# Kernel optimization log

Hardware: AMD Instinct MI355X
Metric: run time of the kernel (lower is better)

The kernel has to match this reference:

```python
import jax, jax.numpy as jnp
import numpy as np
from jax.scipy.special import gammaln

# ---- constants matching init_kwargs ----
D = 64            # num_nodes
K = 64            # DiBS latent rank (k = d default)
P = 32            # n_particles
N_MC = 16         # MC graph samples for score-function grad estimator
PROJ = 128        # proj_dims
N = 2048          # observations
H = 5.0           # h_latent (Frobenius squared-exponential kernel bandwidth)
ALPHA = 0.2       # alpha_linear * t  (single SVGD step)
STEP = 0.005      # SVGD step size
ALPHA_MU = 1.0
ALPHA_LAMBD = float(D + 2)
THETA_MU = 0.0
P_EDGE = 4.0 / (D - 1)          # Erdos-Renyi edge prob (~2 expected edges/node)
LATENT_STD = 1.0 / np.sqrt(K)   # DiBS default latent prior std


def bge_log_marginal(g, data, mu0, alpha_mu, alpha_lambd):
    """BGe log marginal likelihood log p(data | G) for 0/1 adjacency g [d,d]."""
    n, d = data.shape
    small_t = alpha_mu * (alpha_lambd - d - 1.0) / (alpha_mu + 1.0)
    xbar = data.mean(0)
    xc = data - xbar
    R = small_t * jnp.eye(d) + xc.T @ xc \
        + (n * alpha_mu / (n + alpha_mu)) * jnp.outer(xbar - mu0, xbar - mu0)

    def masked_slogdet(mask):  # logdet of R restricted to mask-selected rows/cols
        m = jnp.outer(mask, mask)
        return jnp.linalg.slogdet(m * R + (1.0 - m) * jnp.eye(d))[1]

    def node_score(j):
        parents = g[:, j].astype(R.dtype)
        pj = jnp.maximum(parents, (jnp.arange(d) == j).astype(R.dtype))
        l = jnp.sum(parents)
        log_gamma = (0.5 * (jnp.log(alpha_mu) - jnp.log(n + alpha_mu))
                     + gammaln(0.5 * (n + alpha_lambd - d + l + 1.0))
                     - gammaln(0.5 * (alpha_lambd - d + l + 1.0))
                     - 0.5 * n * jnp.log(jnp.pi)
                     + 0.5 * (alpha_lambd - d + 2.0 * l + 1.0) * jnp.log(small_t))
        return (log_gamma
                + 0.5 * (n + alpha_lambd - d + l) * masked_slogdet(parents)
                - 0.5 * (n + alpha_lambd - d + l + 1.0) * masked_slogdet(pj))

    return jnp.sum(jax.vmap(node_score)(jnp.arange(d)))


def _dense(key, fan_in, fan_out):
    return jax.random.normal(key, (fan_in, fan_out), jnp.float32) * 0.05


def setup_inputs() -> dict:
    key = jax.random.key(0)
    ks = jax.random.split(key, 16)
    return {
        "z_gt": jax.random.normal(ks[0], (N, D), jnp.float32),
        "init_particles_z": jax.random.normal(ks[1], (P, D, K, 2), jnp.float32) * LATENT_STD,
        "enc_w0": _dense(ks[2], D * D, 20), "enc_b0": jnp.zeros(20, jnp.float32),
        "enc_w1": _dense(ks[3], 20, D),     "enc_b1": jnp.zeros(D, jnp.float32),
        "enc_w2": _dense(ks[4], D, D),      "enc_b2": jnp.zeros(D, jnp.float32),
        "mu_w0": _dense(ks[5], D, D), "mu_b0": jnp.zeros(D, jnp.float32),
        "mu_w1": _dense(ks[6], D, D), "mu_b1": jnp.zeros(D, jnp.float32),
        "lv_w0": _dense(ks[7], D, D), "lv_b0": jnp.zeros(D, jnp.float32),
        "lv_w1": _dense(ks[8], D, D), "lv_b1": jnp.zeros(D, jnp.float32),
        "dec_w0": _dense(ks[9], D, 10),       "dec_b0": jnp.zeros(10, jnp.float32),
        "dec_w1": _dense(ks[10], 10, PROJ),   "dec_b1": jnp.zeros(PROJ, jnp.float32),
        "dec_w2": _dense(ks[11], PROJ, PROJ), "dec_b2": jnp.zeros(PROJ, jnp.float32),
        "seed": 0,
    }


def reference(z_gt, init_particles_z, enc_w0, enc_b0, enc_w1, enc_b1, enc_w2, enc_b2,
              mu_w0, mu_b0, mu_w1, mu_b1, lv_w0, lv_b0, lv_w1, lv_b1,
              dec_w0, dec_b0, dec_w1, dec_b1, dec_w2, dec_b2, seed):
    key = jax.random.key(seed)
    d = z_gt.shape[1]
    od = 1.0 - jnp.eye(d)
    z = init_particles_z                                   # [P,d,k,2]
    u, v = z[..., 0], z[..., 1]
    scores = jnp.einsum('pik,pjk->pij', u, v)              # [P,d,d]
    probs = jax.nn.sigmoid(ALPHA * scores) * od            # soft graph, zero diag

    # --- score-function estimate of grad_z log E_G[p(data|G)] (DiBS marginal) ---
    key, sk = jax.random.split(key)
    gs = jax.random.bernoulli(sk, probs[:, None], (P, N_MC, d, d)).astype(z.dtype) * od
    mu0_inf = jnp.zeros(d, z.dtype)
    logp = jax.vmap(jax.vmap(
        lambda g: bge_log_marginal(g, z_gt, mu0_inf, 1.0, d + 2.0)))(gs)   # [P,S]
    w = jax.nn.softmax(logp, axis=1)                       # self-normalized weights
    M = ALPHA * (gs - probs[:, None]) * od                 # d log q(G|Z) / d scores
    grad_u = jnp.einsum('ps,psij,pjk->pik', w, M, v)
    grad_v = jnp.einsum('ps,psij,pik->pjk', w, M, u)

    # --- grad of soft-graph ER prior + Gaussian latent prior ---
    logit_pe = jnp.log(P_EDGE) - jnp.log1p(-P_EDGE)
    Mp = ALPHA * probs * (1.0 - probs) * logit_pe * od
    grad_u = grad_u + jnp.einsum('pij,pjk->pik', Mp, v) - u / (LATENT_STD ** 2)
    grad_v = grad_v + jnp.einsum('pij,pik->pjk', Mp, u) - v / (LATENT_STD ** 2)
    grads = jnp.stack([grad_u, grad_v], axis=-1)           # [P,d,k,2]

    # --- one SVGD step with Frobenius squared-exponential kernel ---
    zf = z.reshape(P, -1)
    gf = grads.reshape(P, -1)
    sq = jnp.sum((zf[:, None] - zf[None]) ** 2, -1)
    Kmat = jnp.exp(-sq / H)                                # symmetric [P,P]
    rep = (-2.0 / H) * (Kmat @ zf - zf * Kmat.sum(1, keepdims=True))
    z_new = z + STEP * ((Kmat @ gf + rep) / P).reshape(z.shape)

    # --- hard graphs: particle_to_g_lim (alpha -> inf) ---
    s2 = jnp.einsum('pik,pjk->pij', z_new[..., 0], z_new[..., 1])
    g_hard = (s2 > 0).astype(z.dtype) * od                 # [P,d,d]

    mu0_bge = jnp.full(d, THETA_MU, z.dtype)
    log_p_z_given_g = jax.vmap(
        lambda g: bge_log_marginal(g, z_gt, mu0_bge, ALPHA_MU, ALPHA_LAMBD))(g_hard)

    # --- q(z | G) encoder (batched over particles) ---
    gf2 = g_hard.reshape(g_hard.shape[0], d * d)
    h = jax.nn.relu(gf2 @ enc_w0 + enc_b0)
    h = jax.nn.relu(h @ enc_w1 + enc_b1)
    h = jax.nn.relu(h @ enc_w2 + enc_b2)
    q_mu = jax.nn.relu(h @ mu_w0 + mu_b0) @ mu_w1 + mu_b1
    q_lv = jax.nn.relu(h @ lv_w0 + lv_b0) @ lv_w1 + lv_b1

    key, rk = jax.random.split(key)
    eps = jax.random.normal(rk, q_lv.shape, q_lv.dtype)
    q_z = q_mu + eps * jnp.exp(0.5 * q_lv)                 # reparameterize

    # --- decoder ---
    hdec = jax.nn.relu(q_z @ dec_w0 + dec_b0)
    hdec = jax.nn.relu(hdec @ dec_w1 + dec_b1)
    recons = hdec @ dec_w2 + dec_b2                        # [P, PROJ]

    return recons, log_p_z_given_g, q_z, q_mu, q_lv, g_hard, z_new
```

## Files before the change

### kernel.cpp

```cpp
#include <hip/hip_runtime.h>
#include <stdint.h>
#include <math.h>

typedef unsigned long long u64;
typedef unsigned int u32;
typedef unsigned short u16;

#define C_P 32
#define C_S 16
#define C_D 64
#define C_N 2048

#define R_OFF      0
#define CTAB_OFF   4160
#define KEYS_OFF   4224
#define PROBS_OFF  4232
#define GROW_OFF   135304
#define GCOL_OFF   168072
#define NS_OFF     200840
#define W_OFF      233608
#define GF_OFF     234120
#define KM_OFF     365192
#define ZN_OFF     365704
#define NS2_OFF    496776

#define WL_LIST0 16

#define HBLK 768
#define TB1 1280
#define TB0 2112
#define TB2 1312
#define E_H  (HBLK)
#define E_1  (E_H + TB1)
#define E_0  (E_1 + TB0)
#define NBLK_ALL (E_0 + TB2)

#define O_REC   0
#define O_LOGP  4096
#define O_QZ    4128
#define O_QMU   6176
#define O_QLV   8224
#define O_GH    10272
#define O_ZN    141344
#define O_TOTAL 403488

__device__ __forceinline__ void tf2x32(u32 k0, u32 k1, u32 x0, u32 x1,
                                       u32& o0, u32& o1) {
  u32 ks2 = k0 ^ k1 ^ 0x1BD11BDAu;
  x0 += k0; x1 += k1;
#define TFR(r) { x0 += x1; x1 = (x1 << r) | (x1 >> (32 - r)); x1 ^= x0; }
  TFR(13) TFR(15) TFR(26) TFR(6)   x0 += k1;  x1 += ks2 + 1u;
  TFR(17) TFR(29) TFR(16) TFR(24)  x0 += ks2; x1 += k0 + 2u;
  TFR(13) TFR(15) TFR(26) TFR(6)   x0 += k0;  x1 += k1 + 3u;
  TFR(17) TFR(29) TFR(16) TFR(24)  x0 += k1;  x1 += ks2 + 4u;
  TFR(13) TFR(15) TFR(26) TFR(6)   x0 += ks2; x1 += k0 + 5u;
#undef TFR
  o0 = x0; o1 = x1;
}

__device__ __forceinline__ double d_erfinv(double x) {
  double w = -log1p(-x * x);
  double p;
  if (w < 5.0) {
    w -= 2.5;
    p = 2.81022636e-08;
    p = 3.43273939e-07  + p * w;
    p = -3.5233877e-06  + p * w;
    p = -4.39150654e-06 + p * w;
    p = 0.00021858087   + p * w;
    p = -0.00125372503  + p * w;
    p = -0.00417768164  + p * w;
    p = 0.246640727     + p * w;
    p = 1.50140941      + p * w;
  } else {
    w = sqrt(w) - 3.0;
    p = -0.000200214257;
    p = 0.000100950558  + p * w;
    p = 0.00134934322   + p * w;
    p = -0.00367342844  + p * w;
    p = 0.00573950773   + p * w;
    p = -0.0076224613   + p * w;
    p = 0.00943887047   + p * w;
    p = 1.00167406      + p * w;
    p = 2.83297682      + p * w;
  }
  return p * x;
}

__device__ __forceinline__ double stirl(double z) {
  double zi = 1.0 / z;
  double zi2 = zi * zi;
  double s = (z - 0.5) * log(z) - z + 0.9189385332046727;
  s += zi * (1.0 / 12.0 - zi2 * (1.0 / 360.0 - zi2 * (1.0 / 1260.0)));
  return s;
}

__global__ void k_init(const float* x, const float* z, double* ws, const int* seedp) {
  int t = threadIdx.x;
  if (blockIdx.x < 64) {
    __shared__ double pS[8][64], pX[8][64];
    __shared__ double xbar[64];
    int j = blockIdx.x;
    int i = t & 63, c = t >> 6;
    if (j == 0) {
      if (t < 64) {
        int l = t;
        double term = (l >= 2) ? log((2049.0 + (double)l) / (4.0 * (1.0 + (double)l)))
                               : 0.0;
        double v = term;
#pragma unroll
        for (int off = 2; off <= 32; off <<= 1) {
          double o = __shfl_up(v, off, 64);
          if (l >= off) v += o;
        }
        const double LOG_HALF = -0.6931471805599453;
        double c0 = -0.5 * log(2049.0)
                  - 1024.0 * log(3.14159265358979323846);
        double seed = (l & 1)
          ? c0 + stirl(1026.0) + 2.5 * LOG_HALF
          : c0 + stirl(1025.5) + 0.12078223763524522235 + 1.5 * LOG_HALF;
        ws[CTAB_OFF + l] = seed + v;
      }
      if (t < 8) ((u32*)(ws + GF_OFF))[t] = 0;
      if (t == 0) {
        u32 kk0 = 0u, kk1 = (u32)seedp[0];
        u32 a0, a1, s0, s1, r0, r1, d0, d1;
        tf2x32(kk0, kk1, 0u, 0u, a0, a1);
        tf2x32(kk0, kk1, 0u, 1u, s0, s1);
        tf2x32(a0, a1, 0u, 0u, d0, d1); (void)d0; (void)d1;
        tf2x32(a0, a1, 0u, 1u, r0, r1);
        u32* keys = (u32*)(ws + KEYS_OFF);
        keys[0] = s0; keys[1] = s1; keys[2] = r0; keys[3] = r1;
      }
    }
    double sx = 0.0, sxx = 0.0;
    for (int n = c * 256; n < (c + 1) * 256; n++) {
      double xi = (double)x[n * 64 + i];
      double xj = (double)x[n * 64 + j];
      sx += xi; sxx += xi * xj;
    }
    pS[c][i] = sx; pX[c][i] = sxx;
    __syncthreads();
    if (t < 64) {
      double S = 0.0, X = 0.0;
      for (int cc = 0; cc < 8; cc++) { S += pS[cc][i]; X += pX[cc][i]; }
      xbar[i] = S / 2048.0;
      pX[0][i] = X;
    }
    __syncthreads();
    if (t < 64) {
      double xbi = xbar[i], xbj = xbar[j];
      double s = pX[0][i] - 2048.0 * xbi * xbj + (2048.0 / 2049.0) * xbi * xbj;
      if (i == j) s += 0.5;
      ((float*)(ws + R_OFF))[i * 64 + j] = (float)s;
    }
  } else {
    __shared__ float V[64 * 65];
    __shared__ float us[8][64];
    float* probs = (float*)(ws + PROBS_OFF);
    int b2 = blockIdx.x - 64;
    int p = b2 >> 3;
    int i = (b2 & 7) * 8 + (t >> 6);
    int j = t & 63, w = t >> 6;
    for (int jj = w; jj < 64; jj += 8)
      V[jj * 65 + j] = z[((p * 64 + jj) * 64 + j) * 2 + 1];
    us[w][j] = z[((p * 64 + i) * 64 + j) * 2 + 0];
    __syncthreads();
    float s = 0.f;
    for (int kk = 0; kk < 64; kk++)
      s += us[w][kk] * V[j * 65 + kk];
    float pr = (i == j) ? 0.f : 1.f / (1.f + expf(-0.2f * s));
    probs[(p * 64 + i) * 64 + j] = pr;
  }
}

__global__ void k_sample(double* ws) {
  const float* probs = (const float*)(ws + PROBS_OFF);
  const u32* keys = (const u32*)(ws + KEYS_OFF);
  u64* grow = (u64*)(ws + GROW_OFF);
  u64* gcol = (u64*)(ws + GCOL_OFF);
  u32* wl = (u32*)(ws + GF_OFF);
  int ps = blockIdx.x;
  int p = ps >> 4;
  int j = threadIdx.x;
  u32 k0 = keys[0], k1 = keys[1];
  u64 colmask = 0;
  for (int i = 0; i < 64; i++) {
    u32 lin = (u32)(ps * 4096 + i * 64 + j);
    u32 o0, o1; tf2x32(k0, k1, 0u, lin, o0, o1);
    u32 bits = o0 ^ o1;
    float f = __uint_as_float((bits >> 9) | 0x3f800000u) - 1.0f;
    bool bit = (f < probs[(p * 64 + i) * 64 + j]);
    u64 rm = __ballot(bit);
    if (j == 0) grow[ps * 64 + i] = rm;
    if (bit) colmask |= (1ull << i);
  }
  gcol[ps * 64 + j] = colmask;
  int m = (int)__popcll(colmask) + 1;
  int tier = (m <= 32) ? 0 : (m <= 36) ? 1 : (m <= 40) ? 2 : 3;
#pragma unroll
  for (int t = 0; t < 4; t++) {
    u64 b = __ballot(tier == t);
    if (tier == t) {
      int leader = (int)__builtin_ctzll(b);
      u32 off = (u32)__popcll(b & ((1ull << j) - 1ull));
      u32 base = 0;
      if (j == leader) base = atomicAdd(&wl[t], (u32)__popcll(b));
      base = (u32)__shfl((int)base, leader, 64);
      wl[WL_LIST0 + t * 32768 + base + off] = (u32)(ps * 64 + j);
    }
  }
}

__device__ __forceinline__ float rdlane(float x, int l) {
  return __uint_as_float(__builtin_amdgcn_readlane(__float_as_uint(x), (u32)l));
}

template<int MMAX>
__device__ __forceinline__ void tier_body2(const float* Rf, const double* ctab,
                                           const u64* masks, double* nodescore,
                                           const u32* wl, int tier,
                                           u32 brel, u32 nb, int (*idx)[2][64]) {
  int w = threadIdx.x >> 6;
  int lane = threadIdx.x & 63;
  u32 cnt = wl[tier];
  const u32* list = wl + WL_LIST0 + tier * 32768;
  u32 npair = (cnt + 1) >> 1;
  for (u32 ti = brel * 4 + (u32)w; ti < npair; ti += nb * 4) {
    u32 iA = 2 * ti, iB = iA + 1;
    bool hasB = (iB < cnt);
    int taskA = (int)list[iA];
    int taskB = (int)list[hasB ? iB : iA];
    u64 maskA = masks[taskA];
    u64 maskB = masks[taskB];
    int PA = (int)__popcll(maskA), PB = (int)__popcll(maskB);
    idx[w][0][lane] = 0;
    idx[w][1][lane] = 0;
    __builtin_amdgcn_wave_barrier();
    {
      u64 belowA = maskA & ((1ull << lane) - 1ull);
      if ((maskA >> lane) & 1ull) idx[w][0][(int)__popcll(belowA)] = lane;
      if (lane == 0) idx[w][0][PA] = taskA & 63;
      u64 belowB = maskB & ((1ull << lane) - 1ull);
      if ((maskB >> lane) & 1ull) idx[w][1][(int)__popcll(belowB)] = lane;
      if (lane == 0) idx[w][1][PB] = taskB & 63;
    }
    __builtin_amdgcn_wave_barrier();
    int rowA = idx[w][0][lane];
    int rowB = idx[w][1][lane];
    float va[MMAX], vb[MMAX];
#pragma unroll
    for (int c = 0; c < MMAX; c++) {
      va[c] = Rf[idx[w][0][c] * 64 + rowA];
      vb[c] = Rf[idx[w][1][c] * 64 + rowB];
    }
    float pivA = 1.0f, pivB = 1.0f;
#pragma unroll
    for (int k = 0; k < MMAX; k++) {
      float dkA = rdlane(va[k], k);
      float dkB = rdlane(vb[k], k);
      if (lane == k) { pivA = dkA; pivB = dkB; }
      float nsA = -va[k] * __builtin_amdgcn_rcpf(dkA);
      float nsB = -vb[k] * __builtin_amdgcn_rcpf(dkB);
#pragma unroll
      for (int b2 = k + 1; b2 < MMAX; b2++) {
        va[b2] += nsA * rdlane(va[k], b2);
        vb[b2] += nsB * rdlane(vb[k], b2);
      }
    }
    {
      int mA = PA + 1;
      float lastd = __shfl(pivA, PA, 64);
      float lv = (lane < mA) ? __logf(pivA) : 0.f;
      for (int off = 32; off > 0; off >>= 1) lv += __shfl_down(lv, off, 64);
      if (lane == 0) {
        double l = (double)PA;
        nodescore[taskA] = ctab[PA]
                         - 0.5 * (2050.0 + l) * (double)__logf(lastd)
                         - 0.5 * (double)lv;
      }
    }
    if (hasB) {
      int mB = PB + 1;
      float lastd = __shfl(pivB, PB, 64);
      float lv = (lane < mB) ? __logf(pivB) : 0.f;
      for (int off = 32; off > 0; off >>= 1) lv += __shfl_down(lv, off, 64);
      if (lane == 0) {
        double l = (double)PB;
        nodescore[taskB] = ctab[PB]
                         - 0.5 * (2050.0 + l) * (double)__logf(lastd)
                         - 0.5 * (double)lv;
      }
    }
    __builtin_amdgcn_wave_barrier();
  }
}

template<int MMAX>
__device__ __forceinline__ void tier_body(const float* Rf, const double* ctab,
                                          const u64* masks, double* nodescore,
                                          const u32* wl, int tier,
                                          u32 brel, u32 nb, int (*idx)[64]) {
  int w = threadIdx.x >> 6;
  int lane = threadIdx.x & 63;
  u32 cnt = wl[tier];
  const u32* list = wl + WL_LIST0 + tier * 32768;
  for (u32 ti = brel * 4 + (u32)w; ti < cnt; ti += nb * 4) {
    int task = (int)list[ti];
    int j = task & 63;
    u64 mask = masks[task];
    int P = (int)__popcll(mask);
    int m = P + 1;
    idx[w][lane] = 0;
    __builtin_amdgcn_wave_barrier();
    u64 below = mask & ((1ull << lane) - 1ull);
    if ((mask >> lane) & 1ull) idx[w][(int)__popcll(below)] = lane;
    if (lane == 0) idx[w][P] = j;
    __builtin_amdgcn_wave_barrier();
    int myrow = idx[w][lane];
    float v[MMAX];
#pragma unroll
    for (int c = 0; c < MMAX; c++)
      v[c] = Rf[idx[w][c] * 64 + myrow];
    float mypiv = 1.0f;
#pragma unroll
    for (int k = 0; k < MMAX; k++) {
      if (k < m) {
        float dk = rdlane(v[k], k);
        if (lane == k) mypiv = dk;
        float ns = -v[k] * __builtin_amdgcn_rcpf(dk);
#pragma unroll
        for (int b = k + 1; b < MMAX; b++)
          v[b] += ns * rdlane(v[k], b);
      }
    }
    float lastd = __shfl(mypiv, P, 64);
    float lv = (lane < m) ? __logf(mypiv) : 0.f;
    for (int off = 32; off > 0; off >>= 1) lv += __shfl_down(lv, off, 64);
    if (lane == 0) {
      double l = (double)P;
      nodescore[task] = ctab[P]
                      - 0.5 * (2050.0 + l) * (double)__logf(lastd)
                      - 0.5 * (double)lv;
    }
    __builtin_amdgcn_wave_barrier();
  }
}

#define WB() __builtin_amdgcn_wave_barrier()

__device__ void heavy_body(const float* Rf, const double* ctab,
                           const u64* masks, double* nodescore,
                           const u32* wl, u32 brel, u32 nb,
                           float* T, int* idx) {
  if (threadIdx.x >= 64) return;
  int lane = threadIdx.x;
  u32 cnt = wl[3];
  const u32* list = wl + WL_LIST0 + 3 * 32768;
  for (u32 ii = brel; ii < cnt; ii += nb) {
    WB();
    int task = (int)list[ii];
    int j = task & 63;
    u64 mask = masks[task];
    int P = (int)__popcll(mask);
    int m = P + 1;
    u64 below = mask & ((1ull << lane) - 1ull);
    if ((mask >> lane) & 1ull) idx[(int)__popcll(below)] = lane;
    if (lane == 0) idx[P] = j;
    WB();
    int trLane = (lane * (lane + 1)) >> 1;
    if (lane < m) {
      int cidx = idx[lane];
      int tr = 0;
      for (int r = 0; r < m; r++) {
        if (lane <= r) T[tr + lane] = Rf[idx[r] * 64 + cidx];
        tr += r + 1;
      }
    }
    WB();
    float mypiv = 1.0f, lastd = 1.0f;
    float v[40];
#pragma unroll
    for (int c = 0; c < 40; c++)
      v[c] = T[trLane + c];
#pragma unroll
    for (int k = 0; k < 40; k++) {
      if (k < m) {
        float dk = rdlane(v[k], k);
        if (lane == k) mypiv = dk;
        lastd = dk;
        float ns = -v[k] * __builtin_amdgcn_rcpf(dk);
#pragma unroll
        for (int b = k + 1; b < 40; b++)
          v[b] += ns * rdlane(v[k], b);
      }
    }
    if (m > 40) {
      for (int b = 40; b < m; b++) {
        float acc = 0.f;
#pragma unroll
        for (int k = 0; k < 40; k++) {
          float dk = rdlane(v[k], k);
          float abk = rdlane(v[k], b);
          acc += v[k] * abk * __builtin_amdgcn_rcpf(dk);
        }
        if (lane >= b) T[trLane + b] -= acc;
      }
      WB();
      for (int k = 40; k < m; k++) {
        float dk = T[((k * (k + 1)) >> 1) + k];
        if (lane == k) mypiv = dk;
        lastd = dk;
        float sk = T[trLane + k] * __builtin_amdgcn_rcpf(dk);
        for (int b = k + 1; b < m; b++) {
          float abk = T[((b * (b + 1)) >> 1) + k];
          if (lane >= b) T[trLane + b] -= sk * abk;
        }
        WB();
      }
    }
    double vv = (lane < m) ? log((double)mypiv) : 0.0;
    for (int off = 32; off > 0; off >>= 1) vv += __shfl_down(vv, off, 64);
    if (lane == 0) {
      double logB = vv;
      double logA = logB - log((double)lastd);
      double l = (double)P;
      nodescore[task] = ctab[P]
                      + 0.5 * (2050.0 + l) * logA
                      - 0.5 * (2051.0 + l) * logB;
    }
  }
}

__global__ __launch_bounds__(256) void k_chol_all(const float* Rf, const double* ctab,
                                                  const u64* masks, double* nodescore,
                                                  const u32* wl) {
  __shared__ int idx2[4][2][64];
  __shared__ int idx4[4][64];
  __shared__ float T[2080];
  __shared__ int idxh[64];
  u32 b = blockIdx.x;
  if (b < E_H)      heavy_body(Rf, ctab, masks, nodescore, wl, b, HBLK, T, idxh);
  else if (b < E_1) tier_body2<36>(Rf, ctab, masks, nodescore, wl, 1, b - E_H, TB1, idx2);
  else if (b < E_0) tier_body2<32>(Rf, ctab, masks, nodescore, wl, 0, b - E_1, TB0, idx2);
  else              tier_body<40>(Rf, ctab, masks, nodescore, wl, 2, b - E_0, TB2, idx4);
}

template<bool TRANSPOSE>
__global__ __launch_bounds__(64) void k_chol(const float* Rf, const double* ctab,
                                             const u64* masks, double* nodescore) {
  __shared__ float T[2080];
  __shared__ int idx[64];
  int task = blockIdx.x;
  int j = task & 63;
  int lane = threadIdx.x;
  u64 mask;
  if (TRANSPOSE) {
    int p = task >> 6;
    u64 rm = masks[p * 64 + lane];
    mask = __ballot((rm >> j) & 1ull);
  } else {
    mask = masks[task];
  }
  int P = (int)__popcll(mask);
  int m = P + 1;
  u64 below = mask & ((1ull << lane) - 1ull);
  if ((mask >> lane) & 1ull) idx[(int)__popcll(below)] = lane;
  if (lane == 0) idx[P] = j;
  __syncthreads();
  int trLane = (lane * (lane + 1)) >> 1;
  if (lane < m) {
    int cidx = idx[lane];
    int tr = 0;
    for (int r = 0; r < m; r++) {
      if (lane <= r) T[tr + lane] = Rf[idx[r] * 64 + cidx];
      tr += r + 1;
    }
  }
  __syncthreads();
  float mypiv = 1.0f, lastd = 1.0f;
  float v[40];
#pragma unroll
  for (int c = 0; c < 40; c++)
    v[c] = T[trLane + c];
#pragma unroll
  for (int k = 0; k < 40; k++) {
    if (k < m) {
      float dk = rdlane(v[k], k);
      if (lane == k) mypiv = dk;
      lastd = dk;
      float ns = -v[k] * __builtin_amdgcn_rcpf(dk);
#pragma unroll
      for (int b = k + 1; b < 40; b++)
        v[b] += ns * rdlane(v[k], b);
    }
  }
  if (m > 40) {
    for (int b = 40; b < m; b++) {
      float acc = 0.f;
#pragma unroll
      for (int k = 0; k < 40; k++) {
        float dk = rdlane(v[k], k);
        float abk = rdlane(v[k], b);
        acc += v[k] * abk * __builtin_amdgcn_rcpf(dk);
      }
      if (lane >= b) T[trLane + b] -= acc;
    }
    __syncthreads();
    for (int k = 40; k < m; k++) {
      float dk = T[((k * (k + 1)) >> 1) + k];
      if (lane == k) mypiv = dk;
      lastd = dk;
      float sk = T[trLane + k] * __builtin_amdgcn_rcpf(dk);
      for (int b = k + 1; b < m; b++) {
        float abk = T[((b * (b + 1)) >> 1) + k];
        if (lane >= b) T[trLane + b] -= sk * abk;
      }
      __syncthreads();
    }
  }
  double vv = (lane < m) ? log((double)mypiv) : 0.0;
  for (int off = 32; off > 0; off >>= 1) vv += __shfl_down(vv, off, 64);
  if (lane == 0) {
    double logB = vv;
    double logA = logB - log((double)lastd);
    double l = (double)P;
    nodescore[task] = ctab[P]
                    + 0.5 * (2050.0 + l) * logA
                    - 0.5 * (2051.0 + l) * logB;
  }
}

__global__ void k_grad(double* ws, const float* z) {
  const float* probs = (const float*)(ws + PROBS_OFF);
  const u64* grow = (const u64*)(ws + GROW_OFF);
  const u64* gcol = (const u64*)(ws + GCOL_OFF);
  const double* ns = ws + NS_OFF;
  float* gf = (float*)(ws + GF_OFF);
  const float LOGIT = -2.6903717578966254f;
  int bb = blockIdx.x;
  int k = threadIdx.x;
  __shared__ float acc[64];
  __shared__ double part[64];
  __shared__ double wsh[16];
  if (bb < 4096) {
    int p = (bb < 2048) ? (bb >> 6) : ((bb - 2048) >> 6);
    {
      int s = k & 15, c = k >> 4;
      double a2 = 0.0;
      for (int j2 = c * 16; j2 < (c + 1) * 16; j2++)
        a2 += ns[(p * 16 + s) * 64 + j2];
      part[k] = a2;
      __syncthreads();
      if (k < 16) part[k] = part[k] + part[k + 16] + part[k + 32] + part[k + 48];
      __syncthreads();
      if (k == 0) {
        double m2 = part[0];
        for (int s2 = 1; s2 < 16; s2++) m2 = fmax(m2, part[s2]);
        double e[16], sum = 0.0;
        for (int s2 = 0; s2 < 16; s2++) { e[s2] = exp(part[s2] - m2); sum += e[s2]; }
        for (int s2 = 0; s2 < 16; s2++) wsh[s2] = e[s2] / sum;
      }
      __syncthreads();
    }
    if (bb < 2048) {
      int i = bb & 63;
      float gb = 0.f, wsum = 0.f;
      for (int s = 0; s < 16; s++) {
        float wv = (float)wsh[s];
        wsum += wv;
        gb += wv * (float)((grow[(p * 16 + s) * 64 + i] >> k) & 1ull);
      }
      float pr = probs[(p * 64 + i) * 64 + k];
      float od = (i == k) ? 0.f : 1.f;
      acc[k] = (0.2f * (gb - pr * wsum) + 0.2f * pr * (1.f - pr) * LOGIT) * od;
      __syncthreads();
      float s = 0.f;
      for (int j = 0; j < 64; j++)
        s += acc[j] * z[((p * 64 + j) * 64 + k) * 2 + 1];
      s -= 64.f * z[((p * 64 + i) * 64 + k) * 2 + 0];
      gf[p * 8192 + (i * 64 + k) * 2 + 0] = s;
    } else {
      int j = (bb - 2048) & 63;
      float gb = 0.f, wsum = 0.f;
      for (int s = 0; s < 16; s++) {
        float wv = (float)wsh[s];
        wsum += wv;
        gb += wv * (float)((gcol[(p * 16 + s) * 64 + j] >> k) & 1ull);
      }
      float pr = probs[(p * 64 + k) * 64 + j];
      float od = (k == j) ? 0.f : 1.f;
      acc[k] = (0.2f * (gb - pr * wsum) + 0.2f * pr * (1.f - pr) * LOGIT) * od;
      __syncthreads();
      float s = 0.f;
      for (int i = 0; i < 64; i++)
        s += acc[i] * z[((p * 64 + i) * 64 + k) * 2 + 0];
      s -= 64.f * z[((p * 64 + j) * 64 + k) * 2 + 1];
      gf[p * 8192 + (j * 64 + k) * 2 + 1] = s;
    }
  } else {
    float* Km = (float*)(ws + KM_OFF);
    int b = bb - 4096;
    int a = b >> 5, b2 = b & 31;
    float accf = 0.f;
    for (int d0 = k; d0 < 8192; d0 += 64) {
      float diff = z[a * 8192 + d0] - z[b2 * 8192 + d0];
      accf += diff * diff;
    }
    for (int off = 32; off > 0; off >>= 1) accf += __shfl_down(accf, off, 64);
    if (k == 0) Km[a * 32 + b2] = expf(-accf / 5.0f);
  }
}

__global__ void k_znew(const float* z, double* ws, float* out) {
  const float* Km = (const float*)(ws + KM_OFF);
  const float* gf = (const float*)(ws + GF_OFF);
  float* zn = (float*)(ws + ZN_OFF);
  int gid = blockIdx.x * 64 + threadIdx.x;
  int p = gid >> 13, t = gid & 8191;
  float zp = z[p * 8192 + t];
  float accg = 0.f, accz = 0.f, ks = 0.f;
  for (int b = 0; b < 32; b++) {
    float kv = Km[p * 32 + b];
    accg += kv * gf[b * 8192 + t];
    accz += kv * z[b * 8192 + t];
    ks += kv;
  }
  float rep = -0.4f * (accz - zp * ks);
  float v = zp + 0.005f * ((accg + rep) / 32.f);
  zn[p * 8192 + t] = v;
  out[O_ZN + p * 8192 + t] = v;
}

__global__ __launch_bounds__(64) void k_s2col(double* ws, float* out) {
  const float* zn = (const float*)(ws + ZN_OFF);
  u64* grow2 = (u64*)(ws + NS_OFF);
  int b = blockIdx.x; int p = b >> 6, i = b & 63;
  int j = threadIdx.x;
  __shared__ float V[64 * 65];
  __shared__ float us[64];
  int k = j;
  us[k] = zn[p * 8192 + (i * 64 + k) * 2 + 0];
  for (int jj = 0; jj < 64; jj++)
    V[jj * 65 + k] = zn[p * 8192 + (jj * 64 + k) * 2 + 1];
  __syncthreads();
  float s = 0.f;
  for (int kk = 0; kk < 64; kk++)
    s += us[kk] * V[j * 65 + kk];
  bool bit = (i != j) && (s > 0.0f);
  out[O_GH + (p * 64 + i) * 64 + j] = bit ? 1.0f : 0.0f;
  u64 m = __ballot(bit);
  if (j == 0) grow2[p * 64 + i] = m;
}

__global__ __launch_bounds__(256) void k_mlp(double* ws, float* out, const double* ns2,
    const float* ew0, const float* eb0, const float* ew1, const float* eb1,
    const float* ew2, const float* eb2,
    const float* mw0, const float* mb0, const float* mw1, const float* mb1,
    const float* lw0, const float* lb0, const float* lw1, const float* lb1,
    const float* dw0, const float* db0, const float* dw1, const float* db1,
    const float* dw2, const float* db2) {
  int p = blockIdx.x, t = threadIdx.x;
  int w = t >> 6, lane = t & 63;
  const u64* grow2 = (const u64*)(ws + NS_OFF);
  const u32* keys = (const u32*)(ws + KEYS_OFF);
  __shared__ float pt[4][64];
  __shared__ float e0p[4][20];
  __shared__ float h0[20], h1[64], h2[64], hm[64], hl[64];
  __shared__ float qmu[64], qlv[64], qz[64], h3[10], h4[128];

  if (w == 0) {
    double vv = ns2[p * 64 + lane];
    for (int off = 32; off > 0; off >>= 1) vv += __shfl_down(vv, off, 64);
    if (lane == 0) out[O_LOGP + p] = (float)vv;
  }

  {
    int i = t >> 2;
    int jb = (t & 3) * 16;
    u32 m16 = (u32)((grow2[p * 64 + i] >> jb) & 0xFFFFull);
    float acc[20];
#pragma unroll
    for (int o = 0; o < 20; o++) acc[o] = 0.f;
    const float4* wb = (const float4*)(ew0 + (size_t)(t * 16) * 20);
#pragma unroll
    for (int q = 0; q < 16; q++) {
      float mq = (float)((m16 >> q) & 1u);
      float4 r0 = wb[q * 5 + 0], r1 = wb[q * 5 + 1], r2 = wb[q * 5 + 2];
      float4 r3 = wb[q * 5 + 3], r4 = wb[q * 5 + 4];
      acc[0]  += mq * r0.x; acc[1]  += mq * r0.y; acc[2]  += mq * r0.z; acc[3]  += mq * r0.w;
      acc[4]  += mq * r1.x; acc[5]  += mq * r1.y; acc[6]  += mq * r1.z; acc[7]  += mq * r1.w;
      acc[8]  += mq * r2.x; acc[9]  += mq * r2.y; acc[10] += mq * r2.z; acc[11] += mq * r2.w;
      acc[12] += mq * r3.x; acc[13] += mq * r3.y; acc[14] += mq * r3.z; acc[15] += mq * r3.w;
      acc[16] += mq * r4.x; acc[17] += mq * r4.y; acc[18] += mq * r4.z; acc[19] += mq * r4.w;
    }
#pragma unroll
    for (int o = 0; o < 20; o++) {
      float v = acc[o];
      for (int off = 32; off > 0; off >>= 1) v += __shfl_down(v, off, 64);
      if (lane == 0) e0p[w][o] = v;
    }
  }
  __syncthreads();
  if (t < 20)
    h0[t] = fmaxf(eb0[t] + e0p[0][t] + e0p[1][t] + e0p[2][t] + e0p[3][t], 0.f);
  __syncthreads();

  {
    float s = 0.f;
#pragma unroll
    for (int q = 0; q < 5; q++) s += h0[w * 5 + q] * ew1[(w * 5 + q) * 64 + lane];
    pt[w][lane] = s;
  }
  __syncthreads();
  if (w == 0)
    h1[lane] = fmaxf(eb1[lane] + pt[0][lane] + pt[1][lane] + pt[2][lane] + pt[3][lane], 0.f);
  __syncthreads();

  {
    float s = 0.f;
#pragma unroll
    for (int q = 0; q < 16; q++) s += h1[w * 16 + q] * ew2[(w * 16 + q) * 64 + lane];
    pt[w][lane] = s;
  }
  __syncthreads();
  if (w == 0)
    h2[lane] = fmaxf(eb2[lane] + pt[0][lane] + pt[1][lane] + pt[2][lane] + pt[3][lane], 0.f);
  __syncthreads();

  {
    const float* W = (w < 2) ? mw0 : lw0;
    int qb = (w & 1) * 32;
    float s = 0.f;
#pragma unroll
    for (int q = 0; q < 32; q++) s += h2[qb + q] * W[(qb + q) * 64 + lane];
    pt[w][lane] = s;
  }
  __syncthreads();
  if (w == 0) hm[lane] = fmaxf(mb0[lane] + pt[0][lane] + pt[1][lane], 0.f);
  if (w == 1) hl[lane] = fmaxf(lb0[lane] + pt[2][lane] + pt[3][lane], 0.f);
  __syncthreads();

  {
    const float* W = (w < 2) ? mw1 : lw1;
    const float* src = (w < 2) ? hm : hl;
    int qb = (w & 1) * 32;
    float s = 0.f;
#pragma unroll
    for (int q = 0; q < 32; q++) s += src[qb + q] * W[(qb + q) * 64 + lane];
    pt[w][lane] = s;
  }
  __syncthreads();
  if (w == 0) qmu[lane] = mb1[lane] + pt[0][lane] + pt[1][lane];
  if (w == 1) qlv[lane] = lb1[lane] + pt[2][lane] + pt[3][lane];
  __syncthreads();

  if (w == 0) {
    u32 o0, o1;
    tf2x32(keys[2], keys[3], 0u, (u32)(p * 64 + lane), o0, o1);
    u32 bits = o0 ^ o1;
    float f = __uint_as_float((bits >> 9) | 0x3f800000u) - 1.0f;
    float LOF = __uint_as_float(0xBF7FFFFFu);
    float uu = fmaxf(LOF, f * 2.0f + LOF);
    float eps = (float)(1.4142135623730951 * d_erfinv((double)uu));
    float qzv = qmu[lane] + eps * expf(0.5f * qlv[lane]);
    qz[lane] = qzv;
    out[O_QZ  + p * 64 + lane] = qzv;
    out[O_QMU + p * 64 + lane] = qmu[lane];
    out[O_QLV + p * 64 + lane] = qlv[lane];
  }
  __syncthreads();

  {
    float s = 0.f;
    if (lane < 10) {
#pragma unroll
      for (int q = 0; q < 16; q++) s += qz[w * 16 + q] * dw0[(w * 16 + q) * 10 + lane];
    }
    pt[w][lane] = s;
  }
  __syncthreads();
  if (w == 0 && lane < 10)
    h3[lane] = fmaxf(db0[lane] + pt[0][lane] + pt[1][lane] + pt[2][lane] + pt[3][lane], 0.f);
  __syncthreads();

  {
    int o = (w >> 1) * 64 + lane;
    int qb = (w & 1) * 5;
    float s = 0.f;
#pragma unroll
    for (int q = 0; q < 5; q++) s += h3[qb + q] * dw1[(qb + q) * 128 + o];
    pt[w][lane] = s;
  }
  __syncthreads();
  if (w == 0) h4[lane]      = fmaxf(db1[lane]      + pt[0][lane] + pt[1][lane], 0.f);
  if (w == 1) h4[64 + lane] = fmaxf(db1[64 + lane] + pt[2][lane] + pt[3][lane], 0.f);
  __syncthreads();

  {
    int o = (w >> 1) * 64 + lane;
    int qb = (w & 1) * 64;
    float s = 0.f;
#pragma unroll
    for (int q = 0; q < 64; q++) s += h4[qb + q] * dw2[(qb + q) * 128 + o];
    pt[w][lane] = s;
  }
  __syncthreads();
  if (w == 0) out[O_REC + p * 128 + lane]      = db2[lane]      + pt[0][lane] + pt[1][lane];
  if (w == 1) out[O_REC + p * 128 + 64 + lane] = db2[64 + lane] + pt[2][lane] + pt[3][lane];
}

extern "C" void kernel_launch(void* const* d_in, const int* in_sizes, int n_in,
                              void* d_out, int out_size, void* d_ws, size_t ws_size,
                              hipStream_t stream) {
  (void)in_sizes; (void)n_in; (void)out_size; (void)ws_size;
  const float* z_gt = (const float*)d_in[0];
  const float* z0   = (const float*)d_in[1];
  const float* ew0 = (const float*)d_in[2];  const float* eb0 = (const float*)d_in[3];
  const float* ew1 = (const float*)d_in[4];  const float* eb1 = (const float*)d_in[5];
  const float* ew2 = (const float*)d_in[6];  const float* eb2 = (const float*)d_in[7];
  const float* mw0 = (const float*)d_in[8];  const float* mb0 = (const float*)d_in[9];
  const float* mw1 = (const float*)d_in[10]; const float* mb1 = (const float*)d_in[11];
  const float* lw0 = (const float*)d_in[12]; const float* lb0 = (const float*)d_in[13];
  const float* lw1 = (const float*)d_in[14]; const float* lb1 = (const float*)d_in[15];
  const float* dw0 = (const float*)d_in[16]; const float* db0 = (const float*)d_in[17];
  const float* dw1 = (const float*)d_in[18]; const float* db1 = (const float*)d_in[19];
  const float* dw2 = (const float*)d_in[20]; const float* db2 = (const float*)d_in[21];
  const int* seed = (const int*)d_in[22];
  double* ws = (double*)d_ws;
  float* out = (float*)d_out;
  const float* Rf = (const float*)(ws + R_OFF);
  const u32* wl = (const u32*)(ws + GF_OFF);

  k_init<<<320, 512, 0, stream>>>(z_gt, z0, ws, seed);
  k_sample<<<C_P * C_S, 64, 0, stream>>>(ws);
  k_chol_all<<<NBLK_ALL, 256, 0, stream>>>(Rf, ws + CTAB_OFF,
      (const u64*)(ws + GCOL_OFF), ws + NS_OFF, wl);
  k_grad<<<2 * C_P * C_D + C_P * C_P, 64, 0, stream>>>(ws, z0);
  k_znew<<<(C_P * 8192) / 64, 64, 0, stream>>>(z0, ws, out);
  k_s2col<<<C_P * C_D, 64, 0, stream>>>(ws, out);
  k_chol<true><<<C_P * C_D, 64, 0, stream>>>(Rf, ws + CTAB_OFF,
      (const u64*)(ws + NS_OFF), ws + NS2_OFF);
  k_mlp<<<C_P, 256, 0, stream>>>(ws, out, ws + NS2_OFF,
      ew0, eb0, ew1, eb1, ew2, eb2,
      mw0, mb0, mw1, mb1, lw0, lb0, lw1, lb1,
      dw0, db0, dw1, db1, dw2, db2);
}
```

Baseline: 329.3 us.

## Fuse graph sampling into init, move kernel matrix into Cholesky launch

The Bernoulli graph-sampling kernel is merged into k_init. Each block now computes a particle's full edge-probability matrix in shared memory and samples 8 MC graphs from it, recomputing the sampling key locally instead of reading it from the workspace. The SVGD kernel-matrix computation moves from k_grad into extra blocks of k_chol_all, and k_s2col switches to 512-thread blocks handling 8 rows each. The aim is fewer launches and less tail latency, at the cost of duplicated probability computation and a hipMemset that replaces the in-kernel worklist reset.

```diff
diff --git a/kernel.cpp b/kernel.cpp
--- a/kernel.cpp
+++ b/kernel.cpp
@@ -33,7 +33,9 @@
 #define E_H  (HBLK)
 #define E_1  (E_H + TB1)
 #define E_0  (E_1 + TB0)
-#define NBLK_ALL (E_0 + TB2)
+#define E_2  (E_0 + TB2)
+#define KMB  256
+#define NBLK_ALL (E_2 + KMB)
 
 #define O_REC   0
 #define O_LOGP  4096
@@ -96,10 +98,12 @@
 }
 
 __global__ void k_init(const float* x, const float* z, double* ws, const int* seedp) {
+  __shared__ double smem[6208];
   int t = threadIdx.x;
   if (blockIdx.x < 64) {
-    __shared__ double pS[8][64], pX[8][64];
-    __shared__ double xbar[64];
+    double* pS = smem;
+    double* pX = smem + 512;
+    double* xbar = smem + 1024;
     int j = blockIdx.x;
     int i = t & 63, c = t >> 6;
     if (j == 0) {
@@ -121,7 +125,6 @@
           : c0 + stirl(1025.5) + 0.12078223763524522235 + 1.5 * LOG_HALF;
         ws[CTAB_OFF + l] = seed + v;
       }
-      if (t < 8) ((u32*)(ws + GF_OFF))[t] = 0;
       if (t == 0) {
         u32 kk0 = 0u, kk1 = (u32)seedp[0];
         u32 a0, a1, s0, s1, r0, r1, d0, d1;
@@ -139,75 +142,76 @@
       double xj = (double)x[n * 64 + j];
       sx += xi; sxx += xi * xj;
     }
-    pS[c][i] = sx; pX[c][i] = sxx;
+    pS[c * 64 + i] = sx; pX[c * 64 + i] = sxx;
     __syncthreads();
     if (t < 64) {
       double S = 0.0, X = 0.0;
-      for (int cc = 0; cc < 8; cc++) { S += pS[cc][i]; X += pX[cc][i]; }
+      for (int cc = 0; cc < 8; cc++) { S += pS[cc * 64 + i]; X += pX[cc * 64 + i]; }
       xbar[i] = S / 2048.0;
-      pX[0][i] = X;
+      pX[i] = X;
     }
     __syncthreads();
     if (t < 64) {
       double xbi = xbar[i], xbj = xbar[j];
-      double s = pX[0][i] - 2048.0 * xbi * xbj + (2048.0 / 2049.0) * xbi * xbj;
+      double s = pX[i] - 2048.0 * xbi * xbj + (2048.0 / 2049.0) * xbi * xbj;
       if (i == j) s += 0.5;
       ((float*)(ws + R_OFF))[i * 64 + j] = (float)s;
     }
   } else {
-    __shared__ float V[64 * 65];
-    __shared__ float us[8][64];
+    float* V  = (float*)smem;
+    float* U  = V + 64 * 65;
+    float* PL = U + 64 * 65;
     float* probs = (float*)(ws + PROBS_OFF);
-    int b2 = blockIdx.x - 64;
-    int p = b2 >> 3;
-    int i = (b2 & 7) * 8 + (t >> 6);
+    u64* grow = (u64*)(ws + GROW_OFF);
+    u64* gcol = (u64*)(ws + GCOL_OFF);
+    u32* wl = (u32*)(ws + GF_OFF);
+    int sidx = blockIdx.x - 64;
+    int p = sidx >> 1, half = sidx & 1;
     int j = t & 63, w = t >> 6;
-    for (int jj = w; jj < 64; jj += 8)
+    for (int jj = w; jj < 64; jj += 8) {
       V[jj * 65 + j] = z[((p * 64 + jj) * 64 + j) * 2 + 1];
-    us[w][j] = z[((p * 64 + i) * 64 + j) * 2 + 0];
-    __syncthreads();
-    float s = 0.f;
-    for (int kk = 0; kk < 64; kk++)
-      s += us[w][kk] * V[j * 65 + kk];
-    float pr = (i == j) ? 0.f : 1.f / (1.f + expf(-0.2f * s));
-    probs[(p * 64 + i) * 64 + j] = pr;
-  }
-}
-
-__global__ void k_sample(double* ws) {
-  const float* probs = (const float*)(ws + PROBS_OFF);
-  const u32* keys = (const u32*)(ws + KEYS_OFF);
-  u64* grow = (u64*)(ws + GROW_OFF);
-  u64* gcol = (u64*)(ws + GCOL_OFF);
-  u32* wl = (u32*)(ws + GF_OFF);
-  int ps = blockIdx.x;
-  int p = ps >> 4;
-  int j = threadIdx.x;
-  u32 k0 = keys[0], k1 = keys[1];
-  u64 colmask = 0;
-  for (int i = 0; i < 64; i++) {
-    u32 lin = (u32)(ps * 4096 + i * 64 + j);
-    u32 o0, o1; tf2x32(k0, k1, 0u, lin, o0, o1);
-    u32 bits = o0 ^ o1;
-    float f = __uint_as_float((bits >> 9) | 0x3f800000u) - 1.0f;
-    bool bit = (f < probs[(p * 64 + i) * 64 + j]);
-    u64 rm = __ballot(bit);
-    if (j == 0) grow[ps * 64 + i] = rm;
-    if (bit) colmask |= (1ull << i);
-  }
-  gcol[ps * 64 + j] = colmask;
-  int m = (int)__popcll(colmask) + 1;
-  int tier = (m <= 32) ? 0 : (m <= 36) ? 1 : (m <= 40) ? 2 : 3;
-#pragma unroll
-  for (int t = 0; t < 4; t++) {
-    u64 b = __ballot(tier == t);
-    if (tier == t) {
-      int leader = (int)__builtin_ctzll(b);
-      u32 off = (u32)__popcll(b & ((1ull << j) - 1ull));
-      u32 base = 0;
-      if (j == leader) base = atomicAdd(&wl[t], (u32)__popcll(b));
-      base = (u32)__shfl((int)base, leader, 64);
-      wl[WL_LIST0 + t * 32768 + base + off] = (u32)(ps * 64 + j);
+      U[jj * 65 + j] = z[((p * 64 + jj) * 64 + j) * 2 + 0];
+    }
+    __syncthreads();
+#pragma unroll
+    for (int r = 0; r < 8; r++) {
+      int i = w * 8 + r;
+      float s = 0.f;
+      for (int kk = 0; kk < 64; kk++)
+        s += U[i * 65 + kk] * V[j * 65 + kk];
+      float pr = (i == j) ? 0.f : 1.f / (1.f + expf(-0.2f * s));
+      PL[i * 64 + j] = pr;
+      if (half == 0) probs[(p * 64 + i) * 64 + j] = pr;
+    }
+    __syncthreads();
+    int ps = p * 16 + half * 8 + w;
+    u32 kk1 = (u32)seedp[0];
+    u32 k0, k1; tf2x32(0u, kk1, 0u, 1u, k0, k1);
+    u64 colmask = 0;
+    for (int i = 0; i < 64; i++) {
+      u32 lin = (u32)(ps * 4096 + i * 64 + j);
+      u32 o0, o1; tf2x32(k0, k1, 0u, lin, o0, o1);
+      u32 bits = o0 ^ o1;
+      float f = __uint_as_float((bits >> 9) | 0x3f800000u) - 1.0f;
+      bool bit = (f < PL[i * 64 + j]);
+      u64 rm = __ballot(bit);
+      if (j == 0) grow[ps * 64 + i] = rm;
+      if (bit) colmask |= (1ull << i);
+    }
+    gcol[ps * 64 + j] = colmask;
+    int m = (int)__popcll(colmask) + 1;
+    int tier = (m <= 32) ? 0 : (m <= 36) ? 1 : (m <= 40) ? 2 : 3;
+#pragma unroll
+    for (int tt = 0; tt < 4; tt++) {
+      u64 b = __ballot(tier == tt);
+      if (tier == tt) {
+        int leader = (int)__builtin_ctzll(b);
+        u32 off = (u32)__popcll(b & ((1ull << j) - 1ull));
+        u32 base = 0;
+        if (j == leader) base = atomicAdd(&wl[tt], (u32)__popcll(b));
+        base = (u32)__shfl((int)base, leader, 64);
+        wl[WL_LIST0 + tt * 32768 + base + off] = (u32)(ps * 64 + j);
+      }
     }
   }
 }
@@ -434,7 +438,8 @@
 
 __global__ __launch_bounds__(256) void k_chol_all(const float* Rf, const double* ctab,
                                                   const u64* masks, double* nodescore,
-                                                  const u32* wl) {
+                                                  const u32* wl, const float* z,
+                                                  float* Km) {
   __shared__ int idx2[4][2][64];
   __shared__ int idx4[4][64];
   __shared__ float T[2080];
@@ -443,7 +448,19 @@
   if (b < E_H)      heavy_body(Rf, ctab, masks, nodescore, wl, b, HBLK, T, idxh);
   else if (b < E_1) tier_body2<36>(Rf, ctab, masks, nodescore, wl, 1, b - E_H, TB1, idx2);
   else if (b < E_0) tier_body2<32>(Rf, ctab, masks, nodescore, wl, 0, b - E_1, TB0, idx2);
-  else              tier_body<40>(Rf, ctab, masks, nodescore, wl, 2, b - E_0, TB2, idx4);
+  else if (b < E_2) tier_body<40>(Rf, ctab, masks, nodescore, wl, 2, b - E_0, TB2, idx4);
+  else {
+    int pair = (int)(b - E_2) * 4 + (threadIdx.x >> 6);
+    int lane = threadIdx.x & 63;
+    int a = pair >> 5, b2 = pair & 31;
+    float accf = 0.f;
+    for (int d0 = lane; d0 < 8192; d0 += 64) {
+      float diff = z[a * 8192 + d0] - z[b2 * 8192 + d0];
+      accf += diff * diff;
+    }
+    for (int off = 32; off > 0; off >>= 1) accf += __shfl_down(accf, off, 64);
+    if (lane == 0) Km[a * 32 + b2] = expf(-accf / 5.0f);
+  }
 }
 
 template<bool TRANSPOSE>
@@ -543,72 +560,59 @@
   __shared__ float acc[64];
   __shared__ double part[64];
   __shared__ double wsh[16];
-  if (bb < 4096) {
-    int p = (bb < 2048) ? (bb >> 6) : ((bb - 2048) >> 6);
-    {
-      int s = k & 15, c = k >> 4;
-      double a2 = 0.0;
-      for (int j2 = c * 16; j2 < (c + 1) * 16; j2++)
-        a2 += ns[(p * 16 + s) * 64 + j2];
-      part[k] = a2;
-      __syncthreads();
-      if (k < 16) part[k] = part[k] + part[k + 16] + part[k + 32] + part[k + 48];
-      __syncthreads();
-      if (k == 0) {
-        double m2 = part[0];
-        for (int s2 = 1; s2 < 16; s2++) m2 = fmax(m2, part[s2]);
-        double e[16], sum = 0.0;
-        for (int s2 = 0; s2 < 16; s2++) { e[s2] = exp(part[s2] - m2); sum += e[s2]; }
-        for (int s2 = 0; s2 < 16; s2++) wsh[s2] = e[s2] / sum;
-      }
-      __syncthreads();
-    }
-    if (bb < 2048) {
-      int i = bb & 63;
-      float gb = 0.f, wsum = 0.f;
-      for (int s = 0; s < 16; s++) {
-        float wv = (float)wsh[s];
-        wsum += wv;
-        gb += wv * (float)((grow[(p * 16 + s) * 64 + i] >> k) & 1ull);
-      }
-      float pr = probs[(p * 64 + i) * 64 + k];
-      float od = (i == k) ? 0.f : 1.f;
-      acc[k] = (0.2f * (gb - pr * wsum) + 0.2f * pr * (1.f - pr) * LOGIT) * od;
-      __syncthreads();
-      float s = 0.f;
-      for (int j = 0; j < 64; j++)
-        s += acc[j] * z[((p * 64 + j) * 64 + k) * 2 + 1];
-      s -= 64.f * z[((p * 64 + i) * 64 + k) * 2 + 0];
-      gf[p * 8192 + (i * 64 + k) * 2 + 0] = s;
-    } else {
-      int j = (bb - 2048) & 63;
-      float gb = 0.f, wsum = 0.f;
-      for (int s = 0; s < 16; s++) {
-        float wv = (float)wsh[s];
-        wsum += wv;
-        gb += wv * (float)((gcol[(p * 16 + s) * 64 + j] >> k) & 1ull);
-      }
-      float pr = probs[(p * 64 + k) * 64 + j];
-      float od = (k == j) ? 0.f : 1.f;
-      acc[k] = (0.2f * (gb - pr * wsum) + 0.2f * pr * (1.f - pr) * LOGIT) * od;
-      __syncthreads();
-      float s = 0.f;
-      for (int i = 0; i < 64; i++)
-        s += acc[i] * z[((p * 64 + i) * 64 + k) * 2 + 0];
-      s -= 64.f * z[((p * 64 + j) * 64 + k) * 2 + 1];
-      gf[p * 8192 + (j * 64 + k) * 2 + 1] = s;
-    }
+  int p = (bb < 2048) ? (bb >> 6) : ((bb - 2048) >> 6);
+  {
+    int s = k & 15, c = k >> 4;
+    double a2 = 0.0;
+    for (int j2 = c * 16; j2 < (c + 1) * 16; j2++)
+      a2 += ns[(p * 16 + s) * 64 + j2];
+    part[k] = a2;
+    __syncthreads();
+    if (k < 16) part[k] = part[k] + part[k + 16] + part[k + 32] + part[k + 48];
+    __syncthreads();
+    if (k == 0) {
+      double m2 = part[0];
+      for (int s2 = 1; s2 < 16; s2++) m2 = fmax(m2, part[s2]);
+      double e[16], sum = 0.0;
+      for (int s2 = 0; s2 < 16; s2++) { e[s2] = exp(part[s2] - m2); sum += e[s2]; }
+      for (int s2 = 0; s2 < 16; s2++) wsh[s2] = e[s2] / sum;
+    }
+    __syncthreads();
+  }
+  if (bb < 2048) {
+    int i = bb & 63;
+    float gb = 0.f, wsum = 0.f;
+    for (int s = 0; s < 16; s++) {
+      float wv = (float)wsh[s];
+      wsum += wv;
+      gb += wv * (float)((grow[(p * 16 + s) * 64 + i] >> k) & 1ull);
+    }
+    float pr = probs[(p * 64 + i) * 64 + k];
+    float od = (i == k) ? 0.f : 1.f;
+    acc[k] = (0.2f * (gb - pr * wsum) + 0.2f * pr * (1.f - pr) * LOGIT) * od;
+    __syncthreads();
+    float s = 0.f;
+    for (int j = 0; j < 64; j++)
+      s += acc[j] * z[((p * 64 + j) * 64 + k) * 2 + 1];
+    s -= 64.f * z[((p * 64 + i) * 64 + k) * 2 + 0];
+    gf[p * 8192 + (i * 64 + k) * 2 + 0] = s;
   } else {
-    float* Km = (float*)(ws + KM_OFF);
-    int b = bb - 4096;
-    int a = b >> 5, b2 = b & 31;
-    float accf = 0.f;
-    for (int d0 = k; d0 < 8192; d0 += 64) {
-      float diff = z[a * 8192 + d0] - z[b2 * 8192 + d0];
-      accf += diff * diff;
-    }
-    for (int off = 32; off > 0; off >>= 1) accf += __shfl_down(accf, off, 64);
-    if (k == 0) Km[a * 32 + b2] = expf(-accf / 5.0f);
+    int j = (bb - 2048) & 63;
+    float gb = 0.f, wsum = 0.f;
+    for (int s = 0; s < 16; s++) {
+      float wv = (float)wsh[s];
+      wsum += wv;
+      gb += wv * (float)((gcol[(p * 16 + s) * 64 + j] >> k) & 1ull);
+    }
+    float pr = probs[(p * 64 + k) * 64 + j];
+    float od = (k == j) ? 0.f : 1.f;
+    acc[k] = (0.2f * (gb - pr * wsum) + 0.2f * pr * (1.f - pr) * LOGIT) * od;
+    __syncthreads();
+    float s = 0.f;
+    for (int i = 0; i < 64; i++)
+      s += acc[i] * z[((p * 64 + i) * 64 + k) * 2 + 0];
+    s -= 64.f * z[((p * 64 + j) * 64 + k) * 2 + 1];
+    gf[p * 8192 + (j * 64 + k) * 2 + 1] = s;
   }
 }
 
@@ -632,21 +636,23 @@
   out[O_ZN + p * 8192 + t] = v;
 }
 
-__global__ __launch_bounds__(64) void k_s2col(double* ws, float* out) {
+__global__ __launch_bounds__(512) void k_s2col(double* ws, float* out) {
   const float* zn = (const float*)(ws + ZN_OFF);
   u64* grow2 = (u64*)(ws + NS_OFF);
-  int b = blockIdx.x; int p = b >> 6, i = b & 63;
-  int j = threadIdx.x;
   __shared__ float V[64 * 65];
-  __shared__ float us[64];
-  int k = j;
-  us[k] = zn[p * 8192 + (i * 64 + k) * 2 + 0];
-  for (int jj = 0; jj < 64; jj++)
-    V[jj * 65 + k] = zn[p * 8192 + (jj * 64 + k) * 2 + 1];
+  __shared__ float us[8][64];
+  int b = blockIdx.x;
+  int p = b >> 3;
+  int t = threadIdx.x;
+  int j = t & 63, w = t >> 6;
+  int i = (b & 7) * 8 + w;
+  for (int jj = w; jj < 64; jj += 8)
+    V[jj * 65 + j] = zn[p * 8192 + (jj * 64 + j) * 2 + 1];
+  us[w][j] = zn[p * 8192 + (i * 64 + j) * 2 + 0];
   __syncthreads();
   float s = 0.f;
   for (int kk = 0; kk < 64; kk++)
-    s += us[kk] * V[j * 65 + kk];
+    s += us[w][kk] * V[j * 65 + kk];
   bool bit = (i != j) && (s > 0.0f);
   out[O_GH + (p * 64 + i) * 64 + j] = bit ? 1.0f : 0.0f;
   u64 m = __ballot(bit);
@@ -832,13 +838,13 @@
   const float* Rf = (const float*)(ws + R_OFF);
   const u32* wl = (const u32*)(ws + GF_OFF);
 
-  k_init<<<320, 512, 0, stream>>>(z_gt, z0, ws, seed);
-  k_sample<<<C_P * C_S, 64, 0, stream>>>(ws);
+  hipMemsetAsync((void*)(ws + GF_OFF), 0, 32, stream);
+  k_init<<<128, 512, 0, stream>>>(z_gt, z0, ws, seed);
   k_chol_all<<<NBLK_ALL, 256, 0, stream>>>(Rf, ws + CTAB_OFF,
-      (const u64*)(ws + GCOL_OFF), ws + NS_OFF, wl);
-  k_grad<<<2 * C_P * C_D + C_P * C_P, 64, 0, stream>>>(ws, z0);
+      (const u64*)(ws + GCOL_OFF), ws + NS_OFF, wl, z0, (float*)(ws + KM_OFF));
+  k_grad<<<2 * C_P * C_D, 64, 0, stream>>>(ws, z0);
   k_znew<<<(C_P * 8192) / 64, 64, 0, stream>>>(z0, ws, out);
-  k_s2col<<<C_P * C_D, 64, 0, stream>>>(ws, out);
+  k_s2col<<<256, 512, 0, stream>>>(ws, out);
   k_chol<true><<<C_P * C_D, 64, 0, stream>>>(Rf, ws + CTAB_OFF,
       (const u64*)(ws + NS_OFF), ws + NS2_OFF);
   k_mlp<<<C_P, 256, 0, stream>>>(ws, out, ws + NS2_OFF,
```

New measurement: 367.5 us. +11.6%, slower.
